# Kernel tuning notes

Measured on AMD Instinct MI355X. Metric: run time of the kernel, lower is better.

The kernel has to match this reference:

```python
import jax, jax.numpy as jnp
import numpy as np

N_NODES = 100000
N_EDGES = 3200000
HIDDEN = 64
NUM_LABELS = 1000
NUM_GRAPHS = 128


def setup_inputs() -> dict:
    key = jax.random.key(0)
    ks = jax.random.split(key, 12)
    node_labels = jax.random.randint(ks[0], (N_NODES,), 0, NUM_LABELS)
    edge_index = jax.random.randint(ks[1], (2, N_EDGES), 0, N_NODES)
    edge_weight = jax.random.uniform(ks[2], (N_EDGES,), dtype=jnp.float32)
    batch = jnp.sort(jax.random.randint(ks[3], (N_NODES,), 0, NUM_GRAPHS))
    s = 1.0 / np.sqrt(HIDDEN)
    emb = jax.random.normal(ks[4], (NUM_LABELS, HIDDEN), dtype=jnp.float32)
    W1 = jax.random.normal(ks[5], (HIDDEN, HIDDEN), dtype=jnp.float32) * s
    b1 = jnp.zeros((HIDDEN,), dtype=jnp.float32)
    W2 = jax.random.normal(ks[6], (HIDDEN, HIDDEN), dtype=jnp.float32) * s
    b2 = jnp.zeros((HIDDEN,), dtype=jnp.float32)
    W3 = jax.random.normal(ks[7], (HIDDEN, HIDDEN), dtype=jnp.float32) * s
    b3 = jnp.zeros((HIDDEN,), dtype=jnp.float32)
    W4 = jax.random.normal(ks[8], (HIDDEN, 1), dtype=jnp.float32) * s
    b4 = jnp.zeros((1,), dtype=jnp.float32)
    return {"node_labels": node_labels, "edge_index": edge_index,
            "edge_weight": edge_weight, "batch": batch, "emb": emb,
            "W1": W1, "b1": b1, "W2": W2, "b2": b2,
            "W3": W3, "b3": b3, "W4": W4, "b4": b4}


def _gcn_conv(x, W, b, src, dst, ew):
    # PyG GCNConv: add self-loops (weight 1), symmetric D^-1/2 normalization.
    h = x @ W                                               # [N, H]
    deg = jax.ops.segment_sum(ew, dst, num_segments=N_NODES) + 1.0  # self-loop
    dinv = jax.lax.rsqrt(deg)                               # [N]
    norm = dinv[src] * ew * dinv[dst]                       # [E]
    out = jax.ops.segment_sum(h[src] * norm[:, None], dst, num_segments=N_NODES)
    out = out + h * (dinv * dinv)[:, None]                  # self-loop message
    return out + b


def reference(node_labels, edge_index, edge_weight, batch, emb,
              W1, b1, W2, b2, W3, b3, W4, b4):
    src, dst = edge_index[0], edge_index[1]
    x = emb[node_labels]                                    # [N, H]
    x = jax.nn.relu(_gcn_conv(x, W1, b1, src, dst, edge_weight))
    x = jax.nn.relu(_gcn_conv(x, W2, b2, src, dst, edge_weight))
    # global mean pool over graphs (dropout is identity in eval mode)
    sums = jax.ops.segment_sum(x, batch, num_segments=NUM_GRAPHS)   # [G, H]
    cnts = jax.ops.segment_sum(jnp.ones((N_NODES,), x.dtype), batch,
                               num_segments=NUM_GRAPHS)
    g = sums / jnp.maximum(cnts, 1.0)[:, None]
    g = jax.nn.relu(g @ W3 + b3)
    return jnp.squeeze(g @ W4 + b4, axis=-1)                # [G]
```

## Files before the change

### kernel.cpp

```cpp
#include <hip/hip_runtime.h>
#include <hip/hip_fp16.h>

#define N_NODES    100000
#define N_EDGES    3200000
#define HIDDEN     64
#define NUM_GRAPHS 128
#define NUM_LABELS 1000

#define BKT_SHIFT  8
#define NPB        256
#define NBKT       ((N_NODES + NPB - 1) / NPB)
#define CHUNK      8192
#define NBLK_E     ((N_EDGES + CHUNK - 1) / CHUNK)
#define ENTCAP     8960
#define BSLOT      ENTCAP

__global__ void zero_int_kernel(int* __restrict__ p, int n) {
    int i = blockIdx.x * blockDim.x + threadIdx.x;
    if (i < n) p[i] = 0;
}

__global__ __launch_bounds__(256) void bucket_scatter_kernel(
    const int* __restrict__ src, const int* __restrict__ dst,
    const float* __restrict__ ew, int* __restrict__ bktCur,
    int2* __restrict__ barr, int E) {
    __shared__ int h[NBKT];
    __shared__ int wbase[NBKT];
    int t = threadIdx.x;
    for (int b = t; b < NBKT; b += 256) h[b] = 0;
    __syncthreads();
    int base = blockIdx.x * CHUNK;
    int end  = min(base + CHUNK, E);
    for (int i = base + t; i < end; i += 256)
        atomicAdd(&h[dst[i] >> BKT_SHIFT], 1);
    __syncthreads();
    for (int b = t; b < NBKT; b += 256) {
        int c = h[b];
        wbase[b] = c ? atomicAdd(&bktCur[b], c) : 0;
    }
    __syncthreads();
    for (int b = t; b < NBKT; b += 256) h[b] = 0;
    __syncthreads();
    for (int i = base + t; i < end; i += 256) {
        int d = dst[i];
        int bk = d >> BKT_SHIFT;
        int p = atomicAdd(&h[bk], 1);
        barr[(size_t)bk * BSLOT + wbase[bk] + p] =
            make_int2(src[i] | ((d & (NPB - 1)) << 20), __float_as_int(ew[i]));
    }
}

__global__ __launch_bounds__(512) void scan_buckets_kernel(const int* __restrict__ bktCur,
                                                           int* __restrict__ boff) {
    __shared__ int a[512], b[512];
    int t = threadIdx.x;
    int v = (t < NBKT) ? bktCur[t] : 0;
    a[t] = v; __syncthreads();
    int* pa = a; int* pb = b;
    #pragma unroll
    for (int d = 1; d < 512; d <<= 1) {
        int x = pa[t];
        if (t >= d) x += pa[t - d];
        pb[t] = x; __syncthreads();
        int* tmp = pa; pa = pb; pb = tmp;
    }
    int ex = (t == 0) ? 0 : pa[t - 1];
    if (t < NBKT) boff[t] = ex;
    if (t == NBKT - 1) boff[NBKT] = pa[t];
}

__global__ __launch_bounds__(256) void finalize_kernel(
    const int2* __restrict__ barr, const int* __restrict__ boff,
    const int* __restrict__ labels,
    int2* __restrict__ csr, int* __restrict__ off, float* __restrict__ dinv) {
    __shared__ int2  ent[ENTCAP];
    __shared__ int   hcnt[NPB];
    __shared__ float wsum[NPB];
    __shared__ float ldv[NPB];
    __shared__ int   ha[NPB], hcur[NPB];
    int b = blockIdx.x;
    int t = threadIdx.x;
    int s = boff[b], e = boff[b + 1];
    int m = e - s;
    const int2* bsrc = barr + (size_t)b * BSLOT;
    int node0 = b << BKT_SHIFT;
    int nn = min(NPB, N_NODES - node0);
    if (t < NPB) { hcnt[t] = 0; wsum[t] = 0.f; }
    __syncthreads();
    bool staged = (m <= ENTCAP);
    for (int i = t; i < m; i += 256) {
        int2 v = bsrc[i];
        if (staged) ent[i] = v;
        int doff = (v.x >> 20) & (NPB - 1);
        atomicAdd(&hcnt[doff], 1);
        atomicAdd(&wsum[doff], __int_as_float(v.y));
    }
    __syncthreads();
    ha[t] = hcnt[t];
    __syncthreads();
    #pragma unroll
    for (int d = 1; d < NPB; d <<= 1) {
        int x = ha[t];
        if (t >= d) x += ha[t - d];
        __syncthreads();
        ha[t] = x;
        __syncthreads();
    }
    {
        int ex = (t == 0) ? 0 : ha[t - 1];
        hcur[t] = s + ex;
        float dv = rsqrtf(wsum[t] + 1.0f);
        ldv[t] = dv;
        if (t < nn) {
            off[node0 + t]  = s + ex;
            dinv[node0 + t] = dv;
        }
    }
    if (b == NBKT - 1 && t == 0) off[N_NODES] = e;
    __syncthreads();
    for (int i = t; i < m; i += 256) {
        int2 v = staged ? ent[i] : bsrc[i];
        int doff = (v.x >> 20) & (NPB - 1);
        int sv   = v.x & 0xFFFFF;
        float wf = __int_as_float(v.y) * ldv[doff];
        int lab  = labels[sv];
        int p = atomicAdd(&hcur[doff], 1);
        csr[p] = make_int2(sv | (lab << 17), __float_as_int(wf));
    }
}

__global__ __launch_bounds__(256) void ew1_kernel(
    const float* __restrict__ emb, const float* __restrict__ W,
    __half* __restrict__ OUTH) {
    __shared__ float Ws[64 * 64];
    __shared__ float Xs[64 * 65];
    int t = threadIdx.x;
    #pragma unroll
    for (int s = 0; s < 16; ++s) Ws[s * 256 + t] = W[s * 256 + t];
    int r0   = blockIdx.x * 64;
    int lrow = t >> 2;
    int c0   = (t & 3) * 16;
    int grow = r0 + lrow;
    const float* srcrow = (grow < NUM_LABELS) ? (emb + (size_t)grow * HIDDEN) : emb;
    #pragma unroll
    for (int c = 0; c < 16; c += 4) {
        float4 v = *(const float4*)(srcrow + c0 + c);
        Xs[lrow * 65 + c0 + c + 0] = v.x;
        Xs[lrow * 65 + c0 + c + 1] = v.y;
        Xs[lrow * 65 + c0 + c + 2] = v.z;
        Xs[lrow * 65 + c0 + c + 3] = v.w;
    }
    __syncthreads();
    int row = t & 63;
    int j0  = (t >> 6) * 16;
    float4 a0 = make_float4(0,0,0,0), a1 = a0, a2 = a0, a3 = a0;
    #pragma unroll
    for (int k = 0; k < 64; ++k) {
        float xv = Xs[row * 65 + k];
        const float4* wr = (const float4*)(Ws + k * 64 + j0);
        float4 w0 = wr[0], w1 = wr[1], w2 = wr[2], w3 = wr[3];
        a0.x = fmaf(xv, w0.x, a0.x); a0.y = fmaf(xv, w0.y, a0.y);
        a0.z = fmaf(xv, w0.z, a0.z); a0.w = fmaf(xv, w0.w, a0.w);
        a1.x = fmaf(xv, w1.x, a1.x); a1.y = fmaf(xv, w1.y, a1.y);
        a1.z = fmaf(xv, w1.z, a1.z); a1.w = fmaf(xv, w1.w, a1.w);
        a2.x = fmaf(xv, w2.x, a2.x); a2.y = fmaf(xv, w2.y, a2.y);
        a2.z = fmaf(xv, w2.z, a2.z); a2.w = fmaf(xv, w2.w, a2.w);
        a3.x = fmaf(xv, w3.x, a3.x); a3.y = fmaf(xv, w3.y, a3.y);
        a3.z = fmaf(xv, w3.z, a3.z); a3.w = fmaf(xv, w3.w, a3.w);
    }
    int gr = r0 + row;
    if (gr < NUM_LABELS) {
        union { __half2 h2[8]; uint4 u4[2]; } pk;
        pk.h2[0] = __floats2half2_rn(a0.x, a0.y);
        pk.h2[1] = __floats2half2_rn(a0.z, a0.w);
        pk.h2[2] = __floats2half2_rn(a1.x, a1.y);
        pk.h2[3] = __floats2half2_rn(a1.z, a1.w);
        pk.h2[4] = __floats2half2_rn(a2.x, a2.y);
        pk.h2[5] = __floats2half2_rn(a2.z, a2.w);
        pk.h2[6] = __floats2half2_rn(a3.x, a3.y);
        pk.h2[7] = __floats2half2_rn(a3.z, a3.w);
        uint4* o = (uint4*)(OUTH + (size_t)gr * HIDDEN + j0);
        o[0] = pk.u4[0]; o[1] = pk.u4[1];
    }
}

#define ACC8(rv_, wv_) { \
    const __half2* hp_ = (const __half2*)&(rv_); \
    float2 f0_ = __half22float2(hp_[0]); \
    float2 f1_ = __half22float2(hp_[1]); \
    float2 f2_ = __half22float2(hp_[2]); \
    float2 f3_ = __half22float2(hp_[3]); \
    accA.x = fmaf(f0_.x, (wv_), accA.x); accA.y = fmaf(f0_.y, (wv_), accA.y); \
    accA.z = fmaf(f1_.x, (wv_), accA.z); accA.w = fmaf(f1_.y, (wv_), accA.w); \
    accB.x = fmaf(f2_.x, (wv_), accB.x); accB.y = fmaf(f2_.y, (wv_), accB.y); \
    accB.z = fmaf(f3_.x, (wv_), accB.z); accB.w = fmaf(f3_.y, (wv_), accB.w); }

#define RED8(of_) { \
    accA.x += __shfl_xor(accA.x, of_, 64); accA.y += __shfl_xor(accA.y, of_, 64); \
    accA.z += __shfl_xor(accA.z, of_, 64); accA.w += __shfl_xor(accA.w, of_, 64); \
    accB.x += __shfl_xor(accB.x, of_, 64); accB.y += __shfl_xor(accB.y, of_, 64); \
    accB.z += __shfl_xor(accB.z, of_, 64); accB.w += __shfl_xor(accB.w, of_, 64); }

__global__ __launch_bounds__(256) void agg1_kernel(
    const __half* __restrict__ EW1h, const int* __restrict__ labels,
    const int2* __restrict__ csr, const int* __restrict__ off,
    const float* __restrict__ dinv, const float* __restrict__ bias,
    __half* __restrict__ A1h, int n) {
    int wid  = (blockIdx.x * blockDim.x + threadIdx.x) >> 6;
    if (wid >= n) return;
    int lane = threadIdx.x & 63;
    int q = lane & 7, g = lane >> 3;
    int i   = off[wid] + g;
    int end = off[wid + 1];
    float4 accA = make_float4(0.f,0.f,0.f,0.f), accB = accA;
    while (i < end) {
        int2 e0 = csr[i];
        int2 e1 = (i + 8  < end) ? csr[i + 8]  : make_int2(0, 0);
        int2 e2 = (i + 16 < end) ? csr[i + 16] : make_int2(0, 0);
        int2 e3 = (i + 24 < end) ? csr[i + 24] : make_int2(0, 0);
        uint4 r0 = *(const uint4*)(EW1h + (size_t)((unsigned)e0.x >> 17) * HIDDEN + q * 8);
        uint4 r1 = *(const uint4*)(EW1h + (size_t)((unsigned)e1.x >> 17) * HIDDEN + q * 8);
        uint4 r2 = *(const uint4*)(EW1h + (size_t)((unsigned)e2.x >> 17) * HIDDEN + q * 8);
        uint4 r3 = *(const uint4*)(EW1h + (size_t)((unsigned)e3.x >> 17) * HIDDEN + q * 8);
        float w0 = __int_as_float(e0.y) * dinv[e0.x & 0x1FFFF];
        float w1 = __int_as_float(e1.y) * dinv[e1.x & 0x1FFFF];
        float w2 = __int_as_float(e2.y) * dinv[e2.x & 0x1FFFF];
        float w3 = __int_as_float(e3.y) * dinv[e3.x & 0x1FFFF];
        ACC8(r0, w0); ACC8(r1, w1); ACC8(r2, w2); ACC8(r3, w3);
        i += 32;
    }
    RED8(8); RED8(16); RED8(32);
    if (g == 0) {
        float di  = dinv[wid];
        float di2 = di * di;
        int labw = labels[wid];
        uint4 xu = *(const uint4*)(EW1h + (size_t)labw * HIDDEN + q * 8);
        const __half2* xp = (const __half2*)&xu;
        float2 x0 = __half22float2(xp[0]);
        float2 x1 = __half22float2(xp[1]);
        float2 x2 = __half22float2(xp[2]);
        float2 x3 = __half22float2(xp[3]);
        const float4* bp = (const float4*)(bias + q * 8);
        float4 bv0 = bp[0], bv1 = bp[1];
        float4 vA, vB;
        vA.x = fmaxf(fmaf(x0.x, di2, accA.x) + bv0.x, 0.f);
        vA.y = fmaxf(fmaf(x0.y, di2, accA.y) + bv0.y, 0.f);
        vA.z = fmaxf(fmaf(x1.x, di2, accA.z) + bv0.z, 0.f);
        vA.w = fmaxf(fmaf(x1.y, di2, accA.w) + bv0.w, 0.f);
        vB.x = fmaxf(fmaf(x2.x, di2, accB.x) + bv1.x, 0.f);
        vB.y = fmaxf(fmaf(x2.y, di2, accB.y) + bv1.y, 0.f);
        vB.z = fmaxf(fmaf(x3.x, di2, accB.z) + bv1.z, 0.f);
        vB.w = fmaxf(fmaf(x3.y, di2, accB.w) + bv1.w, 0.f);
        union { __half2 h2[4]; uint4 u4; } pk;
        pk.h2[0] = __floats2half2_rn(vA.x, vA.y);
        pk.h2[1] = __floats2half2_rn(vA.z, vA.w);
        pk.h2[2] = __floats2half2_rn(vB.x, vB.y);
        pk.h2[3] = __floats2half2_rn(vB.z, vB.w);
        *(uint4*)(A1h + (size_t)wid * HIDDEN + q * 8) = pk.u4;
    }
}

__global__ __launch_bounds__(256) void agg2_kernel(
    const __half* __restrict__ Xh,
    const int2* __restrict__ csr, const int* __restrict__ off,
    const float* __restrict__ dinv, float* __restrict__ OUT, int n) {
    int wid  = (blockIdx.x * blockDim.x + threadIdx.x) >> 6;
    if (wid >= n) return;
    int lane = threadIdx.x & 63;
    int q = lane & 7, g = lane >> 3;
    int i   = off[wid] + g;
    int end = off[wid + 1];
    float4 accA = make_float4(0.f,0.f,0.f,0.f), accB = accA;
    while (i < end) {
        int2 e0 = csr[i];
        int2 e1 = (i + 8  < end) ? csr[i + 8]  : make_int2(0, 0);
        int2 e2 = (i + 16 < end) ? csr[i + 16] : make_int2(0, 0);
        int2 e3 = (i + 24 < end) ? csr[i + 24] : make_int2(0, 0);
        uint4 r0 = *(const uint4*)(Xh + (size_t)(e0.x & 0x1FFFF) * HIDDEN + q * 8);
        uint4 r1 = *(const uint4*)(Xh + (size_t)(e1.x & 0x1FFFF) * HIDDEN + q * 8);
        uint4 r2 = *(const uint4*)(Xh + (size_t)(e2.x & 0x1FFFF) * HIDDEN + q * 8);
        uint4 r3 = *(const uint4*)(Xh + (size_t)(e3.x & 0x1FFFF) * HIDDEN + q * 8);
        float w0 = __int_as_float(e0.y) * dinv[e0.x & 0x1FFFF];
        float w1 = __int_as_float(e1.y) * dinv[e1.x & 0x1FFFF];
        float w2 = __int_as_float(e2.y) * dinv[e2.x & 0x1FFFF];
        float w3 = __int_as_float(e3.y) * dinv[e3.x & 0x1FFFF];
        ACC8(r0, w0); ACC8(r1, w1); ACC8(r2, w2); ACC8(r3, w3);
        i += 32;
    }
    RED8(8); RED8(16); RED8(32);
    if (g == 0) {
        float di  = dinv[wid];
        float di2 = di * di;
        uint4 xu = *(const uint4*)(Xh + (size_t)wid * HIDDEN + q * 8);
        const __half2* xp = (const __half2*)&xu;
        float2 x0 = __half22float2(xp[0]);
        float2 x1 = __half22float2(xp[1]);
        float2 x2 = __half22float2(xp[2]);
        float2 x3 = __half22float2(xp[3]);
        accA.x = fmaf(x0.x, di2, accA.x);
        accA.y = fmaf(x0.y, di2, accA.y);
        accA.z = fmaf(x1.x, di2, accA.z);
        accA.w = fmaf(x1.y, di2, accA.w);
        accB.x = fmaf(x2.x, di2, accB.x);
        accB.y = fmaf(x2.y, di2, accB.y);
        accB.z = fmaf(x3.x, di2, accB.z);
        accB.w = fmaf(x3.y, di2, accB.w);
        float* o = OUT + (size_t)wid * HIDDEN + q * 8;
        *(float4*)o       = accA;
        *(float4*)(o + 4) = accB;
    }
}

__global__ __launch_bounds__(256) void gemm2_kernel(
    const float* __restrict__ X, const float* __restrict__ W,
    const float* __restrict__ bias, float* __restrict__ OUT, int n) {
    __shared__ float Ws[64 * 64];
    __shared__ float Xs[64 * 65];
    int t = threadIdx.x;
    #pragma unroll
    for (int s = 0; s < 16; ++s) Ws[s * 256 + t] = W[s * 256 + t];
    int r0   = blockIdx.x * 64;
    int lrow = t >> 2;
    int c0   = (t & 3) * 16;
    const float* srcrow = ((r0 + lrow) < n) ? (X + (size_t)(r0 + lrow) * HIDDEN) : X;
    #pragma unroll
    for (int c = 0; c < 16; c += 4) {
        float4 v = *(const float4*)(srcrow + c0 + c);
        Xs[lrow * 65 + c0 + c + 0] = v.x;
        Xs[lrow * 65 + c0 + c + 1] = v.y;
        Xs[lrow * 65 + c0 + c + 2] = v.z;
        Xs[lrow * 65 + c0 + c + 3] = v.w;
    }
    __syncthreads();
    int row = t & 63;
    int j0  = (t >> 6) * 16;
    float4 a0 = *(const float4*)(bias + j0 + 0);
    float4 a1 = *(const float4*)(bias + j0 + 4);
    float4 a2 = *(const float4*)(bias + j0 + 8);
    float4 a3 = *(const float4*)(bias + j0 + 12);
    #pragma unroll
    for (int k = 0; k < 64; ++k) {
        float xv = Xs[row * 65 + k];
        const float4* wr = (const float4*)(Ws + k * 64 + j0);
        float4 w0 = wr[0], w1 = wr[1], w2 = wr[2], w3 = wr[3];
        a0.x = fmaf(xv, w0.x, a0.x); a0.y = fmaf(xv, w0.y, a0.y);
        a0.z = fmaf(xv, w0.z, a0.z); a0.w = fmaf(xv, w0.w, a0.w);
        a1.x = fmaf(xv, w1.x, a1.x); a1.y = fmaf(xv, w1.y, a1.y);
        a1.z = fmaf(xv, w1.z, a1.z); a1.w = fmaf(xv, w1.w, a1.w);
        a2.x = fmaf(xv, w2.x, a2.x); a2.y = fmaf(xv, w2.y, a2.y);
        a2.z = fmaf(xv, w2.z, a2.z); a2.w = fmaf(xv, w2.w, a2.w);
        a3.x = fmaf(xv, w3.x, a3.x); a3.y = fmaf(xv, w3.y, a3.y);
        a3.z = fmaf(xv, w3.z, a3.z); a3.w = fmaf(xv, w3.w, a3.w);
    }
    int gr = r0 + row;
    if (gr < n) {
        float4* o = (float4*)(OUT + (size_t)gr * HIDDEN + j0);
        a0.x = fmaxf(a0.x, 0.f); a0.y = fmaxf(a0.y, 0.f); a0.z = fmaxf(a0.z, 0.f); a0.w = fmaxf(a0.w, 0.f);
        a1.x = fmaxf(a1.x, 0.f); a1.y = fmaxf(a1.y, 0.f); a1.z = fmaxf(a1.z, 0.f); a1.w = fmaxf(a1.w, 0.f);
        a2.x = fmaxf(a2.x, 0.f); a2.y = fmaxf(a2.y, 0.f); a2.z = fmaxf(a2.z, 0.f); a2.w = fmaxf(a2.w, 0.f);
        a3.x = fmaxf(a3.x, 0.f); a3.y = fmaxf(a3.y, 0.f); a3.z = fmaxf(a3.z, 0.f); a3.w = fmaxf(a3.w, 0.f);
        o[0] = a0; o[1] = a1; o[2] = a2; o[3] = a3;
    }
}

__global__ __launch_bounds__(256) void pool_head_kernel(
    const float* __restrict__ A, const int* __restrict__ batch,
    const float* __restrict__ W3, const float* __restrict__ b3,
    const float* __restrict__ W4, const float* __restrict__ b4,
    float* __restrict__ out) {
    __shared__ int   sb[2];
    __shared__ float sd[4][64];
    __shared__ float gv[64];
    int gidx = blockIdx.x;
    int t = threadIdx.x;
    if (t < 2) {
        int target = gidx + t;
        int lo = 0, hi = N_NODES;
        while (lo < hi) {
            int mid = (lo + hi) >> 1;
            if (batch[mid] < target) lo = mid + 1; else hi = mid;
        }
        sb[t] = lo;
    }
    __syncthreads();
    int start = sb[0], end = sb[1];
    int col = t & 63, rg = t >> 6;
    float sum = 0.f;
    for (int r = start + rg; r < end; r += 4) sum += A[(size_t)r * HIDDEN + col];
    sd[rg][col] = sum;
    __syncthreads();
    if (t < 64) {
        float tot = sd[0][col] + sd[1][col] + sd[2][col] + sd[3][col];
        float cnt = (float)(end - start);
        gv[col] = tot / fmaxf(cnt, 1.0f);
    }
    __syncthreads();
    if (t < 64) {
        float acc = b3[t];
        #pragma unroll
        for (int k = 0; k < 64; ++k) acc = fmaf(gv[k], W3[k * 64 + t], acc);
        float p = fmaxf(acc, 0.f) * W4[t];
        #pragma unroll
        for (int o = 32; o > 0; o >>= 1) p += __shfl_down(p, o, 64);
        if (t == 0) out[gidx] = p + b4[0];
    }
}

extern "C" void kernel_launch(void* const* d_in, const int* in_sizes, int n_in,
                              void* d_out, int out_size, void* d_ws, size_t ws_size,
                              hipStream_t stream) {
    const int*   labels = (const int*)d_in[0];
    const int*   ei     = (const int*)d_in[1];
    const int*   src    = ei;
    const int*   dst    = ei + N_EDGES;
    const float* ew     = (const float*)d_in[2];
    const int*   batch  = (const int*)d_in[3];
    const float* emb    = (const float*)d_in[4];
    const float* W1 = (const float*)d_in[5],  *b1 = (const float*)d_in[6];
    const float* W2 = (const float*)d_in[7],  *b2 = (const float*)d_in[8];
    const float* W3 = (const float*)d_in[9],  *b3 = (const float*)d_in[10];
    const float* W4 = (const float*)d_in[11], *b4 = (const float*)d_in[12];
    float* out = (float*)d_out;

    float* ws   = (float*)d_ws;
    float* bufH = ws;
    float* bufA = bufH + (size_t)N_NODES * HIDDEN;
    int2*  csr  = (int2*)(bufA + (size_t)N_NODES * HIDDEN);
    int*   boff   = (int*)(csr + N_EDGES);
    int*   bktCur = boff + NBKT + 1;
    int*   off    = bktCur + NBKT;
    float* dinv   = (float*)(off + N_NODES + 1);
    __half* EW1h  = (__half*)(dinv + N_NODES);
    int2*  barr   = (int2*)ws;
    __half* A1h   = (__half*)bufA;
    float* A2     = bufA;

    const int NT = 256;
    const int blkW = (N_NODES * 64 + NT - 1) / NT;
    const int blkG = (N_NODES + 63) / 64;

    zero_int_kernel<<<(NBKT + NT - 1) / NT, NT, 0, stream>>>(bktCur, NBKT);
    bucket_scatter_kernel<<<NBLK_E, NT, 0, stream>>>(src, dst, ew, bktCur, barr, N_EDGES);
    scan_buckets_kernel<<<1, 512, 0, stream>>>(bktCur, boff);
    finalize_kernel<<<NBKT, NT, 0, stream>>>(barr, boff, labels, csr, off, dinv);

    ew1_kernel<<<(NUM_LABELS + 63) / 64, NT, 0, stream>>>(emb, W1, EW1h);
    agg1_kernel<<<blkW, NT, 0, stream>>>(EW1h, labels, csr, off, dinv, b1, A1h, N_NODES);

    agg2_kernel<<<blkW, NT, 0, stream>>>(A1h, csr, off, dinv, bufH, N_NODES);
    gemm2_kernel<<<blkG, NT, 0, stream>>>(bufH, W2, b2, A2, N_NODES);

    pool_head_kernel<<<NUM_GRAPHS, NT, 0, stream>>>(A2, batch, W3, b3, W4, b4, out);
}
```

Baseline: 430.1 us.

## Replace atomic bucket reservation with deterministic per-block histogram and column scan

The fused histogram-plus-scatter kernel, which reserved bucket space through global atomics, is split into separate kernels: a per-block histogram, a per-bucket scan across blocks, the existing bucket scan, and a scatter that uses the precomputed bases. This removes global atomic contention and halves the chunk size for more parallelism. In exchange, dst is read twice and a block-by-bucket count matrix is written and read, which adds a kernel launch and extra memory traffic.

```diff
diff --git a/kernel.cpp b/kernel.cpp
--- a/kernel.cpp
+++ b/kernel.cpp
@@ -10,51 +10,65 @@
 #define BKT_SHIFT  8
 #define NPB        256
 #define NBKT       ((N_NODES + NPB - 1) / NPB)
-#define CHUNK      8192
-#define NBLK_E     ((N_EDGES + CHUNK - 1) / CHUNK)
 #define ENTCAP     8960
 #define BSLOT      ENTCAP
-
-__global__ void zero_int_kernel(int* __restrict__ p, int n) {
-    int i = blockIdx.x * blockDim.x + threadIdx.x;
-    if (i < n) p[i] = 0;
-}
-
-__global__ __launch_bounds__(256) void bucket_scatter_kernel(
-    const int* __restrict__ src, const int* __restrict__ dst,
-    const float* __restrict__ ew, int* __restrict__ bktCur,
-    int2* __restrict__ barr, int E) {
+#define SCHUNK     4096
+#define SNBLK      ((N_EDGES + SCHUNK - 1) / SCHUNK)
+#define CPT        ((SNBLK + 255) / 256)
+
+__global__ __launch_bounds__(256) void hist_blk_kernel(
+    const int* __restrict__ dst, int* __restrict__ cnt, int E) {
     __shared__ int h[NBKT];
-    __shared__ int wbase[NBKT];
     int t = threadIdx.x;
     for (int b = t; b < NBKT; b += 256) h[b] = 0;
     __syncthreads();
-    int base = blockIdx.x * CHUNK;
-    int end  = min(base + CHUNK, E);
+    int base = blockIdx.x * SCHUNK;
+    int end  = min(base + SCHUNK, E);
     for (int i = base + t; i < end; i += 256)
         atomicAdd(&h[dst[i] >> BKT_SHIFT], 1);
     __syncthreads();
-    for (int b = t; b < NBKT; b += 256) {
-        int c = h[b];
-        wbase[b] = c ? atomicAdd(&bktCur[b], c) : 0;
-    }
-    __syncthreads();
-    for (int b = t; b < NBKT; b += 256) h[b] = 0;
-    __syncthreads();
-    for (int i = base + t; i < end; i += 256) {
-        int d = dst[i];
-        int bk = d >> BKT_SHIFT;
-        int p = atomicAdd(&h[bk], 1);
-        barr[(size_t)bk * BSLOT + wbase[bk] + p] =
-            make_int2(src[i] | ((d & (NPB - 1)) << 20), __float_as_int(ew[i]));
-    }
-}
-
-__global__ __launch_bounds__(512) void scan_buckets_kernel(const int* __restrict__ bktCur,
+    int* o = cnt + (size_t)blockIdx.x * NBKT;
+    for (int b = t; b < NBKT; b += 256) o[b] = h[b];
+}
+
+__global__ __launch_bounds__(256) void scan_cols_kernel(
+    const int* __restrict__ cnt, int* __restrict__ basem, int* __restrict__ bktTot) {
+    __shared__ int a[256], bsh[256];
+    int b = blockIdx.x;
+    int t = threadIdx.x;
+    int v[CPT];
+    int loc = 0;
+    int blk0 = t * CPT;
+    #pragma unroll
+    for (int j = 0; j < CPT; ++j) {
+        int blk = blk0 + j;
+        int c = (blk < SNBLK) ? cnt[(size_t)blk * NBKT + b] : 0;
+        v[j] = loc;
+        loc += c;
+    }
+    a[t] = loc; __syncthreads();
+    int* pa = a; int* pb = bsh;
+    #pragma unroll
+    for (int d = 1; d < 256; d <<= 1) {
+        int x = pa[t];
+        if (t >= d) x += pa[t - d];
+        pb[t] = x; __syncthreads();
+        int* tmp = pa; pa = pb; pb = tmp;
+    }
+    int ex = (t == 0) ? 0 : pa[t - 1];
+    #pragma unroll
+    for (int j = 0; j < CPT; ++j) {
+        int blk = blk0 + j;
+        if (blk < SNBLK) basem[(size_t)blk * NBKT + b] = ex + v[j];
+    }
+    if (t == 255) bktTot[b] = pa[255];
+}
+
+__global__ __launch_bounds__(512) void scan_buckets_kernel(const int* __restrict__ bktTot,
                                                            int* __restrict__ boff) {
     __shared__ int a[512], b[512];
     int t = threadIdx.x;
-    int v = (t < NBKT) ? bktCur[t] : 0;
+    int v = (t < NBKT) ? bktTot[t] : 0;
     a[t] = v; __syncthreads();
     int* pa = a; int* pb = b;
     #pragma unroll
@@ -67,6 +81,27 @@
     int ex = (t == 0) ? 0 : pa[t - 1];
     if (t < NBKT) boff[t] = ex;
     if (t == NBKT - 1) boff[NBKT] = pa[t];
+}
+
+__global__ __launch_bounds__(256) void scatter_kernel(
+    const int* __restrict__ src, const int* __restrict__ dst,
+    const float* __restrict__ ew, const int* __restrict__ basem,
+    int2* __restrict__ barr, int E) {
+    __shared__ int h[NBKT];
+    __shared__ int wb[NBKT];
+    int t = threadIdx.x;
+    const int* bm = basem + (size_t)blockIdx.x * NBKT;
+    for (int b = t; b < NBKT; b += 256) { h[b] = 0; wb[b] = bm[b]; }
+    __syncthreads();
+    int base = blockIdx.x * SCHUNK;
+    int end  = min(base + SCHUNK, E);
+    for (int i = base + t; i < end; i += 256) {
+        int d  = dst[i];
+        int bk = d >> BKT_SHIFT;
+        int p  = atomicAdd(&h[bk], 1);
+        barr[(size_t)bk * BSLOT + wb[bk] + p] =
+            make_int2(src[i] | ((d & (NPB - 1)) << 20), __float_as_int(ew[i]));
+    }
 }
 
 __global__ __launch_bounds__(256) void finalize_kernel(
@@ -427,21 +462,24 @@
     float* bufA = bufH + (size_t)N_NODES * HIDDEN;
     int2*  csr  = (int2*)(bufA + (size_t)N_NODES * HIDDEN);
     int*   boff   = (int*)(csr + N_EDGES);
-    int*   bktCur = boff + NBKT + 1;
-    int*   off    = bktCur + NBKT;
+    int*   bktTot = boff + NBKT + 1;
+    int*   off    = bktTot + NBKT;
     float* dinv   = (float*)(off + N_NODES + 1);
     __half* EW1h  = (__half*)(dinv + N_NODES);
     int2*  barr   = (int2*)ws;
     __half* A1h   = (__half*)bufA;
     float* A2     = bufA;
+    int*   cnt    = (int*)csr;
+    int*   basem  = cnt + (size_t)SNBLK * NBKT;
 
     const int NT = 256;
     const int blkW = (N_NODES * 64 + NT - 1) / NT;
     const int blkG = (N_NODES + 63) / 64;
 
-    zero_int_kernel<<<(NBKT + NT - 1) / NT, NT, 0, stream>>>(bktCur, NBKT);
-    bucket_scatter_kernel<<<NBLK_E, NT, 0, stream>>>(src, dst, ew, bktCur, barr, N_EDGES);
-    scan_buckets_kernel<<<1, 512, 0, stream>>>(bktCur, boff);
+    hist_blk_kernel<<<SNBLK, NT, 0, stream>>>(dst, cnt, N_EDGES);
+    scan_cols_kernel<<<NBKT, NT, 0, stream>>>(cnt, basem, bktTot);
+    scan_buckets_kernel<<<1, 512, 0, stream>>>(bktTot, boff);
+    scatter_kernel<<<SNBLK, NT, 0, stream>>>(src, dst, ew, basem, barr, N_EDGES);
     finalize_kernel<<<NBKT, NT, 0, stream>>>(barr, boff, labels, csr, off, dinv);
 
     ew1_kernel<<<(NUM_LABELS + 63) / 64, NT, 0, stream>>>(emb, W1, EW1h);
```

After: 413.7 us. 1.04x faster.
